# Optimization experiments

Hardware: AMD Instinct MI355X
Metric: run time of the kernel (lower is better)

The kernel has to match this reference:

```python
import jax, jax.numpy as jnp
import numpy as np

DIM = 1024
N_HEADS = 16

def setup_inputs() -> dict:
    key = jax.random.key(0)
    ks = jax.random.split(key, 6)
    s = 1.0 / np.sqrt(DIM)
    return {
        "x": jax.random.normal(ks[0], (2, 2048, DIM), dtype=jnp.float32),
        "Wq": jax.random.normal(ks[1], (DIM, DIM), dtype=jnp.float32) * s,
        "Wk": jax.random.normal(ks[2], (DIM, DIM), dtype=jnp.float32) * s,
        "Wv": jax.random.normal(ks[3], (DIM, DIM), dtype=jnp.float32) * s,
        "Wo": jax.random.normal(ks[4], (DIM, DIM), dtype=jnp.float32) * s,
        "bo": jax.random.normal(ks[5], (DIM,), dtype=jnp.float32) * 0.01,
    }

def reference(x, Wq, Wk, Wv, Wo, bo):
    B, S, D = x.shape
    H = N_HEADS
    hd = D // H
    # linear layers: y = x @ W.T (torch convention)
    def proj(W):
        y = jnp.einsum('bsd,ed->bse', x, W)
        return y.reshape(B, S, H, hd).transpose(0, 2, 1, 3)  # [B,H,S,hd]
    q, k, v = proj(Wq), proj(Wk), proj(Wv)
    attn = jnp.einsum('bhqd,bhkd->bhqk', q, k) / jnp.sqrt(jnp.float32(hd))
    attn = jax.nn.softmax(attn, axis=-1)
    out = jnp.einsum('bhqk,bhkd->bhqd', attn, v)
    out = out.transpose(0, 2, 1, 3).reshape(B, S, D)
    out = jnp.einsum('bsd,ed->bse', out, Wo) + bo
    return out
```

## Files before the change

kernel.cpp:

```cpp
#include <hip/hip_runtime.h>
#include <hip/hip_bf16.h>

#define SEQ 2048
#define DIM 1024
#define NH 16
#define HD 64
#define MTOT 4096

typedef __attribute__((ext_vector_type(8))) short bf16x8;
typedef __attribute__((ext_vector_type(4))) float f32x4;
typedef __attribute__((ext_vector_type(16))) float f32x16;
typedef __attribute__((ext_vector_type(4))) unsigned int u32x4;
typedef __attribute__((ext_vector_type(2))) unsigned int u32x2;

typedef const __attribute__((address_space(1))) void* gptr_t;
typedef __attribute__((address_space(3))) void* sptr_t;

static __device__ __forceinline__ unsigned short f2bf(float f) {
    unsigned int u = __builtin_bit_cast(unsigned int, f);
    return (unsigned short)((u + 0x7FFFu + ((u >> 16) & 1u)) >> 16);
}

#define CVTPK(d, x, y) asm("v_cvt_pk_bf16_f32 %0, %1, %2" : "=v"(d) : "v"(x), "v"(y))
#define PLSWAP(a, b) asm("v_permlane32_swap_b32 %0, %1" : "+v"(a), "+v"(b))

__global__ void cast_kernel(const float* __restrict__ in, unsigned short* __restrict__ out, int n) {
    int i = (blockIdx.x * 256 + threadIdx.x) * 4;
    if (i < n) {
        float4 v = *reinterpret_cast<const float4*>(in + i);
        ushort4 o;
        o.x = f2bf(v.x); o.y = f2bf(v.y); o.z = f2bf(v.z); o.w = f2bf(v.w);
        *reinterpret_cast<ushort4*>(out + i) = o;
    }
}

template<int MODE>
__global__ __launch_bounds__(256) void gemm_nt(
    const unsigned short* __restrict__ A,
    const unsigned short* __restrict__ B0,
    const unsigned short* __restrict__ B1,
    const unsigned short* __restrict__ B2,
    unsigned short* __restrict__ D0,
    unsigned short* __restrict__ D1,
    unsigned short* __restrict__ D2,
    float* __restrict__ Df,
    const float* __restrict__ bias)
{
    constexpr int K = DIM;
    __shared__ __align__(16) unsigned short Asm[128 * 32];
    __shared__ __align__(16) unsigned short Bsm[128 * 32];

    const int tid = threadIdx.x;
    const int wave = tid >> 6, lane = tid & 63;
    const int wm = wave >> 1, wn = wave & 1;
    const int m0 = blockIdx.y * 128, n0 = blockIdx.x * 128;
    const int fr = lane & 15;

    const unsigned short* Bsel = (MODE == 1 || blockIdx.z == 0) ? B0 : (blockIdx.z == 1 ? B1 : B2);

    const int srow = wave * 32 + (lane >> 2);
    const int schunk = (lane & 3) ^ ((lane >> 3) & 3);
    const size_t abase = (size_t)(m0 + srow) * K + (size_t)schunk * 8;
    const size_t bbase = (size_t)(n0 + srow) * K + (size_t)schunk * 8;

    f32x4 acc[4][4] = {};

    for (int k0 = 0; k0 < K; k0 += 32) {
        #pragma unroll
        for (int c = 0; c < 2; ++c) {
            __builtin_amdgcn_global_load_lds(
                (gptr_t)(A + abase + (size_t)c * 16 * K + k0),
                (sptr_t)((char*)Asm + wave * 2048 + c * 1024), 16, 0, 0);
            __builtin_amdgcn_global_load_lds(
                (gptr_t)(Bsel + bbase + (size_t)c * 16 * K + k0),
                (sptr_t)((char*)Bsm + wave * 2048 + c * 1024), 16, 0, 0);
        }
        __syncthreads();

        bf16x8 af[4], bf[4];
        const int ca = ((lane >> 4) ^ ((fr >> 1) & 3)) * 16;
        #pragma unroll
        for (int i = 0; i < 4; ++i) {
            int ra = wm * 64 + i * 16 + fr;
            int rb = wn * 64 + i * 16 + fr;
            af[i] = *(const bf16x8*)((const char*)Asm + ra * 64 + ca);
            bf[i] = *(const bf16x8*)((const char*)Bsm + rb * 64 + ca);
        }
        #pragma unroll
        for (int i = 0; i < 4; ++i)
            #pragma unroll
            for (int j = 0; j < 4; ++j)
                acc[i][j] = __builtin_amdgcn_mfma_f32_16x16x32_bf16(af[i], bf[j], acc[i][j], 0, 0, 0);
        __syncthreads();
    }

    if (MODE == 0) {
        unsigned short* Dst = (blockIdx.z == 0) ? D0 : (blockIdx.z == 1 ? D1 : D2);
        const float scale = (blockIdx.z == 0) ? 0.1803368787f : 1.0f;
        #pragma unroll
        for (int i = 0; i < 4; ++i)
            #pragma unroll
            for (int j = 0; j < 4; ++j)
                #pragma unroll
                for (int r = 0; r < 4; ++r) {
                    int m = m0 + wm * 64 + i * 16 + (lane >> 4) * 4 + r;
                    int n = n0 + wn * 64 + j * 16 + fr;
                    int b = m >> 11, s = m & 2047, h = n >> 6, dh = n & 63;
                    Dst[(((size_t)(b * NH + h)) * SEQ + s) * HD + dh] = f2bf(acc[i][j][r] * scale);
                }
    } else {
        #pragma unroll
        for (int i = 0; i < 4; ++i)
            #pragma unroll
            for (int j = 0; j < 4; ++j)
                #pragma unroll
                for (int r = 0; r < 4; ++r) {
                    int m = m0 + wm * 64 + i * 16 + (lane >> 4) * 4 + r;
                    int n = n0 + wn * 64 + j * 16 + fr;
                    Df[(size_t)m * DIM + n] = acc[i][j][r] + bias[n];
                }
    }
}

__global__ __launch_bounds__(512, 4) void attn_kernel(
    const unsigned short* __restrict__ Q,
    const unsigned short* __restrict__ Kg,
    const unsigned short* __restrict__ Vg,
    float* __restrict__ po,
    float* __restrict__ ml)
{
    __shared__ __align__(16) unsigned short Ksm[2][64 * 66];
    __shared__ __align__(16) unsigned short Vsm[2][64 * 66];

    const int tid = threadIdx.x;
    const int wave = tid >> 6, lane = tid & 63;
    const int lq = lane & 31, hi = lane >> 5;

    const int bid = blockIdx.x;
    const int xcd = bid & 7, slot = bid >> 3;
    const int bh = xcd * 4 + (slot & 3);
    const int rest = slot >> 2;
    const int q0 = (rest >> 1) * 256;
    const int half = rest & 1;
    const int kvbase = half * 1024;

    const unsigned short* Qh = Q + (size_t)bh * SEQ * HD;
    const unsigned short* Kh = Kg + (size_t)bh * SEQ * HD;
    const unsigned short* Vh = Vg + (size_t)bh * SEQ * HD;

    const float MCONST = 12.0f;

    const int qrow = q0 + wave * 32 + lq;
    bf16x8 qf[4];
    #pragma unroll
    for (int dch = 0; dch < 4; ++dch)
        qf[dch] = *(const bf16x8*)(Qh + (size_t)qrow * HD + dch * 16 + hi * 8);

    f32x16 ot0 = {}, ot1 = {};
    float l = 0.f;

    const int krow_s = tid >> 3, kch_s = tid & 7;
    const int kvp_s = tid >> 4, sub_s = tid & 1;
    const int dch_s = (tid >> 1) & 7;

    bf16x8 sk, sv;
    auto stage_load = [&](int t64) {
        sk = *(const bf16x8*)(Kh + (size_t)(t64 + krow_s) * HD + kch_s * 8);
        sv = *(const bf16x8*)(Vh + (size_t)(t64 + 2 * kvp_s + sub_s) * HD + dch_s * 8);
    };
    auto stage_write = [&](int buf) {
        u32x4 kw = __builtin_bit_cast(u32x4, sk);
        unsigned* kp = (unsigned*)((char*)&Ksm[buf][0] + 132 * krow_s + 16 * kch_s);
        kp[0] = kw[0]; kp[1] = kw[1]; kp[2] = kw[2]; kp[3] = kw[3];
        u32x4 vw = __builtin_bit_cast(u32x4, sv);
        unsigned p0 = (unsigned)__shfl_xor((int)vw[0], 1);
        unsigned p1 = (unsigned)__shfl_xor((int)vw[1], 1);
        unsigned p2 = (unsigned)__shfl_xor((int)vw[2], 1);
        unsigned p3 = (unsigned)__shfl_xor((int)vw[3], 1);
        unsigned ea0 = sub_s ? p2 : vw[0];
        unsigned ea1 = sub_s ? p3 : vw[1];
        unsigned eb0 = sub_s ? vw[2] : p0;
        unsigned eb1 = sub_s ? vw[3] : p1;
        unsigned* vp = (unsigned*)&Vsm[buf][0];
        const int dbase = dch_s * 8 + sub_s * 4;
        vp[33 * (dbase + 0) + kvp_s] = (ea0 & 0xffffu) | (eb0 << 16);
        vp[33 * (dbase + 1) + kvp_s] = (ea0 >> 16) | (eb0 & 0xffff0000u);
        vp[33 * (dbase + 2) + kvp_s] = (ea1 & 0xffffu) | (eb1 << 16);
        vp[33 * (dbase + 3) + kvp_s] = (ea1 >> 16) | (eb1 & 0xffff0000u);
    };

    stage_load(kvbase);
    stage_write(0);
    __syncthreads();

    int cur = 0;
    #pragma unroll 1
    for (int t = 0; t < 16; ++t) {
        if (t < 15) stage_load(kvbase + (t + 1) * 64);

        const char* Kb = (const char*)&Ksm[cur][0];
        const char* Vb = (const char*)&Vsm[cur][0];

        f32x16 st0, st1;
        #pragma unroll
        for (int r = 0; r < 16; ++r) { st0[r] = -MCONST; st1[r] = -MCONST; }
        __builtin_amdgcn_s_setprio(1);
        #pragma unroll
        for (int dch = 0; dch < 4; ++dch) {
            const unsigned* a0 = (const unsigned*)(Kb + 132 * lq + 32 * dch + 16 * hi);
            const unsigned* a1 = (const unsigned*)(Kb + 132 * (32 + lq) + 32 * dch + 16 * hi);
            u32x4 f0 = {a0[0], a0[1], a0[2], a0[3]};
            u32x4 f1 = {a1[0], a1[1], a1[2], a1[3]};
            st0 = __builtin_amdgcn_mfma_f32_32x32x16_bf16(__builtin_bit_cast(bf16x8, f0), qf[dch], st0, 0, 0, 0);
            st1 = __builtin_amdgcn_mfma_f32_32x32x16_bf16(__builtin_bit_cast(bf16x8, f1), qf[dch], st1, 0, 0, 0);
        }
        __builtin_amdgcn_s_setprio(0);

        float sa = 0.f, sb = 0.f, sc = 0.f, sd = 0.f;
        #pragma unroll
        for (int r = 0; r < 16; r += 4) {
            st0[r]     = exp2f(st0[r]);     sa += st0[r];
            st0[r + 1] = exp2f(st0[r + 1]); sb += st0[r + 1];
            st0[r + 2] = exp2f(st0[r + 2]); sc += st0[r + 2];
            st0[r + 3] = exp2f(st0[r + 3]); sd += st0[r + 3];
        }
        #pragma unroll
        for (int r = 0; r < 16; r += 4) {
            st1[r]     = exp2f(st1[r]);     sa += st1[r];
            st1[r + 1] = exp2f(st1[r + 1]); sb += st1[r + 1];
            st1[r + 2] = exp2f(st1[r + 2]); sc += st1[r + 2];
            st1[r + 3] = exp2f(st1[r + 3]); sd += st1[r + 3];
        }
        float ps = (sa + sb) + (sc + sd);
        ps += __shfl_xor(ps, 32);
        l += ps;

        bf16x8 pf0, pf1, pf2, pf3;
        {
            unsigned w0, w1, w2, w3, w4, w5, w6, w7;
            CVTPK(w0, st0[0], st0[1]);   CVTPK(w1, st0[2], st0[3]);
            CVTPK(w2, st0[4], st0[5]);   CVTPK(w3, st0[6], st0[7]);
            CVTPK(w4, st0[8], st0[9]);   CVTPK(w5, st0[10], st0[11]);
            CVTPK(w6, st0[12], st0[13]); CVTPK(w7, st0[14], st0[15]);
            PLSWAP(w0, w2); PLSWAP(w1, w3); PLSWAP(w4, w6); PLSWAP(w5, w7);
            u32x4 uA = {w0, w1, w2, w3}, uB = {w4, w5, w6, w7};
            pf0 = __builtin_bit_cast(bf16x8, uA);
            pf1 = __builtin_bit_cast(bf16x8, uB);
        }
        {
            unsigned w0, w1, w2, w3, w4, w5, w6, w7;
            CVTPK(w0, st1[0], st1[1]);   CVTPK(w1, st1[2], st1[3]);
            CVTPK(w2, st1[4], st1[5]);   CVTPK(w3, st1[6], st1[7]);
            CVTPK(w4, st1[8], st1[9]);   CVTPK(w5, st1[10], st1[11]);
            CVTPK(w6, st1[12], st1[13]); CVTPK(w7, st1[14], st1[15]);
            PLSWAP(w0, w2); PLSWAP(w1, w3); PLSWAP(w4, w6); PLSWAP(w5, w7);
            u32x4 uA = {w0, w1, w2, w3}, uB = {w4, w5, w6, w7};
            pf2 = __builtin_bit_cast(bf16x8, uA);
            pf3 = __builtin_bit_cast(bf16x8, uB);
        }

        __builtin_amdgcn_s_setprio(1);
        #pragma unroll
        for (int kc = 0; kc < 4; ++kc) {
            const unsigned* v0 = (const unsigned*)(Vb + 132 * lq + 32 * kc + 16 * hi);
            const unsigned* v1 = (const unsigned*)(Vb + 132 * (32 + lq) + 32 * kc + 16 * hi);
            u32x4 g0 = {v0[0], v0[1], v0[2], v0[3]};
            u32x4 g1 = {v1[0], v1[1], v1[2], v1[3]};
            bf16x8 pfv = (kc == 0) ? pf0 : (kc == 1) ? pf1 : (kc == 2) ? pf2 : pf3;
            ot0 = __builtin_amdgcn_mfma_f32_32x32x16_bf16(__builtin_bit_cast(bf16x8, g0), pfv, ot0, 0, 0, 0);
            ot1 = __builtin_amdgcn_mfma_f32_32x32x16_bf16(__builtin_bit_cast(bf16x8, g1), pfv, ot1, 0, 0, 0);
        }
        __builtin_amdgcn_s_setprio(0);

        if (t < 15) stage_write(cur ^ 1);
        __syncthreads();
        cur ^= 1;
    }

    const size_t prow = (size_t)(half * 32 + bh) * SEQ + qrow;
    float* por = po + prow * 64;
    #pragma unroll
    for (int tg = 0; tg < 4; ++tg) {
        f32x4 v0 = {ot0[4 * tg + 0], ot0[4 * tg + 1], ot0[4 * tg + 2], ot0[4 * tg + 3]};
        *(f32x4*)(por + 8 * tg + 4 * hi) = v0;
        f32x4 v1 = {ot1[4 * tg + 0], ot1[4 * tg + 1], ot1[4 * tg + 2], ot1[4 * tg + 3]};
        *(f32x4*)(por + 32 + 8 * tg + 4 * hi) = v1;
    }
    if (hi == 0) ml[prow] = l;
}

__global__ __launch_bounds__(256) void merge_kernel(
    const float* __restrict__ po,
    const float* __restrict__ ml,
    unsigned short* __restrict__ ob)
{
    const int gid = blockIdx.x * 256 + threadIdx.x;
    const int row = gid >> 3, dch = gid & 7;
    const size_t p1 = row, p2 = (size_t)32 * SEQ + row;
    const float inv = 1.0f / (ml[p1] + ml[p2]);

    f32x4 a0 = *(const f32x4*)(po + p1 * 64 + dch * 8);
    f32x4 a1 = *(const f32x4*)(po + p1 * 64 + dch * 8 + 4);
    f32x4 b0 = *(const f32x4*)(po + p2 * 64 + dch * 8);
    f32x4 b1 = *(const f32x4*)(po + p2 * 64 + dch * 8 + 4);

    unsigned wA, wB, wC, wD;
    CVTPK(wA, (a0[0] + b0[0]) * inv, (a0[1] + b0[1]) * inv);
    CVTPK(wB, (a0[2] + b0[2]) * inv, (a0[3] + b0[3]) * inv);
    CVTPK(wC, (a1[0] + b1[0]) * inv, (a1[1] + b1[1]) * inv);
    CVTPK(wD, (a1[2] + b1[2]) * inv, (a1[3] + b1[3]) * inv);
    u32x4 w = {wA, wB, wC, wD};

    const int bh = row >> 11, s = row & 2047;
    const int b = bh >> 4, h = bh & 15;
    *(u32x4*)(ob + ((size_t)(b * SEQ + s)) * DIM + h * HD + dch * 8) = w;
}

extern "C" void kernel_launch(void* const* d_in, const int* in_sizes, int n_in,
                              void* d_out, int out_size, void* d_ws, size_t ws_size,
                              hipStream_t stream) {
    const float* x  = (const float*)d_in[0];
    const float* Wq = (const float*)d_in[1];
    const float* Wk = (const float*)d_in[2];
    const float* Wv = (const float*)d_in[3];
    const float* Wo = (const float*)d_in[4];
    const float* bo = (const float*)d_in[5];
    float* out = (float*)d_out;

    unsigned short* ws = (unsigned short*)d_ws;
    unsigned short* xb  = ws;
    unsigned short* wqb = xb + (size_t)MTOT * DIM;
    unsigned short* wkb = wqb + (size_t)DIM * DIM;
    unsigned short* wvb = wkb + (size_t)DIM * DIM;
    unsigned short* wob = wvb + (size_t)DIM * DIM;
    unsigned short* qb  = wob + (size_t)DIM * DIM;
    unsigned short* kb  = qb + (size_t)MTOT * DIM;
    unsigned short* vb  = kb + (size_t)MTOT * DIM;
    unsigned short* ob  = vb + (size_t)MTOT * DIM;
    float* po = (float*)(ob + (size_t)MTOT * DIM);
    float* ml = po + (size_t)2 * 32 * SEQ * 64;

    cast_kernel<<<dim3(MTOT * DIM / 1024), 256, 0, stream>>>(x, xb, MTOT * DIM);
    cast_kernel<<<dim3(DIM * DIM / 1024), 256, 0, stream>>>(Wq, wqb, DIM * DIM);
    cast_kernel<<<dim3(DIM * DIM / 1024), 256, 0, stream>>>(Wk, wkb, DIM * DIM);
    cast_kernel<<<dim3(DIM * DIM / 1024), 256, 0, stream>>>(Wv, wvb, DIM * DIM);
    cast_kernel<<<dim3(DIM * DIM / 1024), 256, 0, stream>>>(Wo, wob, DIM * DIM);

    gemm_nt<0><<<dim3(DIM / 128, MTOT / 128, 3), 256, 0, stream>>>(
        xb, wqb, wkb, wvb, qb, kb, vb, nullptr, nullptr);

    attn_kernel<<<dim3(512), 512, 0, stream>>>(qb, kb, vb, po, ml);

    merge_kernel<<<dim3(2048), 256, 0, stream>>>(po, ml, ob);

    gemm_nt<1><<<dim3(DIM / 128, MTOT / 128, 1), 256, 0, stream>>>(
        ob, wob, nullptr, nullptr, nullptr, nullptr, nullptr, out, bo);
}
```

Before: 144.8 us.

## Process two query row tiles per wave to reuse K/V fragments

Each attention wave now handles 64 query rows (two 32-row tiles) instead of 32, reusing the K and V fragments read from shared memory for both tiles. The grid is halved to 256 blocks with 512-row query chunks, and the launch bound's occupancy hint is lowered to fit the higher register use. This reduces LDS and global K/V traffic per unit of matrix work. The cost is lower occupancy, with only one block per CU, and heavier register pressure.

```diff
diff --git a/kernel.cpp b/kernel.cpp
--- a/kernel.cpp
+++ b/kernel.cpp
@@ -122,7 +122,7 @@
     }
 }
 
-__global__ __launch_bounds__(512, 4) void attn_kernel(
+__global__ __launch_bounds__(512, 2) void attn_kernel(
     const unsigned short* __restrict__ Q,
     const unsigned short* __restrict__ Kg,
     const unsigned short* __restrict__ Vg,
@@ -140,7 +140,7 @@
     const int xcd = bid & 7, slot = bid >> 3;
     const int bh = xcd * 4 + (slot & 3);
     const int rest = slot >> 2;
-    const int q0 = (rest >> 1) * 256;
+    const int q0 = (rest >> 1) * 512;
     const int half = rest & 1;
     const int kvbase = half * 1024;
 
@@ -150,14 +150,17 @@
 
     const float MCONST = 12.0f;
 
-    const int qrow = q0 + wave * 32 + lq;
-    bf16x8 qf[4];
+    const int qrowA = q0 + wave * 64 + lq;
+    const int qrowB = qrowA + 32;
+    bf16x8 qfA[4], qfB[4];
     #pragma unroll
-    for (int dch = 0; dch < 4; ++dch)
-        qf[dch] = *(const bf16x8*)(Qh + (size_t)qrow * HD + dch * 16 + hi * 8);
-
-    f32x16 ot0 = {}, ot1 = {};
-    float l = 0.f;
+    for (int dch = 0; dch < 4; ++dch) {
+        qfA[dch] = *(const bf16x8*)(Qh + (size_t)qrowA * HD + dch * 16 + hi * 8);
+        qfB[dch] = *(const bf16x8*)(Qh + (size_t)qrowB * HD + dch * 16 + hi * 8);
+    }
+
+    f32x16 oA0 = {}, oA1 = {}, oB0 = {}, oB1 = {};
+    float lA = 0.f, lB = 0.f;
 
     const int krow_s = tid >> 3, kch_s = tid & 7;
     const int kvp_s = tid >> 4, sub_s = tid & 1;
@@ -201,62 +204,113 @@
         const char* Kb = (const char*)&Ksm[cur][0];
         const char* Vb = (const char*)&Vsm[cur][0];
 
-        f32x16 st0, st1;
-        #pragma unroll
-        for (int r = 0; r < 16; ++r) { st0[r] = -MCONST; st1[r] = -MCONST; }
-        __builtin_amdgcn_s_setprio(1);
+        bf16x8 kf0[4], kf1[4];
         #pragma unroll
         for (int dch = 0; dch < 4; ++dch) {
             const unsigned* a0 = (const unsigned*)(Kb + 132 * lq + 32 * dch + 16 * hi);
             const unsigned* a1 = (const unsigned*)(Kb + 132 * (32 + lq) + 32 * dch + 16 * hi);
             u32x4 f0 = {a0[0], a0[1], a0[2], a0[3]};
             u32x4 f1 = {a1[0], a1[1], a1[2], a1[3]};
-            st0 = __builtin_amdgcn_mfma_f32_32x32x16_bf16(__builtin_bit_cast(bf16x8, f0), qf[dch], st0, 0, 0, 0);
-            st1 = __builtin_amdgcn_mfma_f32_32x32x16_bf16(__builtin_bit_cast(bf16x8, f1), qf[dch], st1, 0, 0, 0);
-        }
-        __builtin_amdgcn_s_setprio(0);
-
-        float sa = 0.f, sb = 0.f, sc = 0.f, sd = 0.f;
-        #pragma unroll
-        for (int r = 0; r < 16; r += 4) {
-            st0[r]     = exp2f(st0[r]);     sa += st0[r];
-            st0[r + 1] = exp2f(st0[r + 1]); sb += st0[r + 1];
-            st0[r + 2] = exp2f(st0[r + 2]); sc += st0[r + 2];
-            st0[r + 3] = exp2f(st0[r + 3]); sd += st0[r + 3];
-        }
-        #pragma unroll
-        for (int r = 0; r < 16; r += 4) {
-            st1[r]     = exp2f(st1[r]);     sa += st1[r];
-            st1[r + 1] = exp2f(st1[r + 1]); sb += st1[r + 1];
-            st1[r + 2] = exp2f(st1[r + 2]); sc += st1[r + 2];
-            st1[r + 3] = exp2f(st1[r + 3]); sd += st1[r + 3];
-        }
-        float ps = (sa + sb) + (sc + sd);
-        ps += __shfl_xor(ps, 32);
-        l += ps;
-
-        bf16x8 pf0, pf1, pf2, pf3;
+            kf0[dch] = __builtin_bit_cast(bf16x8, f0);
+            kf1[dch] = __builtin_bit_cast(bf16x8, f1);
+        }
+
+        bf16x8 pfA[4], pfB[4];
+
         {
+            f32x16 s0, s1;
+            #pragma unroll
+            for (int r = 0; r < 16; ++r) { s0[r] = -MCONST; s1[r] = -MCONST; }
+            __builtin_amdgcn_s_setprio(1);
+            #pragma unroll
+            for (int dch = 0; dch < 4; ++dch) {
+                s0 = __builtin_amdgcn_mfma_f32_32x32x16_bf16(kf0[dch], qfA[dch], s0, 0, 0, 0);
+                s1 = __builtin_amdgcn_mfma_f32_32x32x16_bf16(kf1[dch], qfA[dch], s1, 0, 0, 0);
+            }
+            __builtin_amdgcn_s_setprio(0);
+            float sa = 0.f, sb = 0.f, sc = 0.f, sd = 0.f;
+            #pragma unroll
+            for (int r = 0; r < 16; r += 4) {
+                s0[r]     = exp2f(s0[r]);     sa += s0[r];
+                s0[r + 1] = exp2f(s0[r + 1]); sb += s0[r + 1];
+                s0[r + 2] = exp2f(s0[r + 2]); sc += s0[r + 2];
+                s0[r + 3] = exp2f(s0[r + 3]); sd += s0[r + 3];
+            }
+            #pragma unroll
+            for (int r = 0; r < 16; r += 4) {
+                s1[r]     = exp2f(s1[r]);     sa += s1[r];
+                s1[r + 1] = exp2f(s1[r + 1]); sb += s1[r + 1];
+                s1[r + 2] = exp2f(s1[r + 2]); sc += s1[r + 2];
+                s1[r + 3] = exp2f(s1[r + 3]); sd += s1[r + 3];
+            }
+            float ps = (sa + sb) + (sc + sd);
+            ps += __shfl_xor(ps, 32);
+            lA += ps;
             unsigned w0, w1, w2, w3, w4, w5, w6, w7;
-            CVTPK(w0, st0[0], st0[1]);   CVTPK(w1, st0[2], st0[3]);
-            CVTPK(w2, st0[4], st0[5]);   CVTPK(w3, st0[6], st0[7]);
-            CVTPK(w4, st0[8], st0[9]);   CVTPK(w5, st0[10], st0[11]);
-            CVTPK(w6, st0[12], st0[13]); CVTPK(w7, st0[14], st0[15]);
+            CVTPK(w0, s0[0], s0[1]);   CVTPK(w1, s0[2], s0[3]);
+            CVTPK(w2, s0[4], s0[5]);   CVTPK(w3, s0[6], s0[7]);
+            CVTPK(w4, s0[8], s0[9]);   CVTPK(w5, s0[10], s0[11]);
+            CVTPK(w6, s0[12], s0[13]); CVTPK(w7, s0[14], s0[15]);
             PLSWAP(w0, w2); PLSWAP(w1, w3); PLSWAP(w4, w6); PLSWAP(w5, w7);
             u32x4 uA = {w0, w1, w2, w3}, uB = {w4, w5, w6, w7};
-            pf0 = __builtin_bit_cast(bf16x8, uA);
-            pf1 = __builtin_bit_cast(bf16x8, uB);
-        }
+            pfA[0] = __builtin_bit_cast(bf16x8, uA);
+            pfA[1] = __builtin_bit_cast(bf16x8, uB);
+            CVTPK(w0, s1[0], s1[1]);   CVTPK(w1, s1[2], s1[3]);
+            CVTPK(w2, s1[4], s1[5]);   CVTPK(w3, s1[6], s1[7]);
+            CVTPK(w4, s1[8], s1[9]);   CVTPK(w5, s1[10], s1[11]);
+            CVTPK(w6, s1[12], s1[13]); CVTPK(w7, s1[14], s1[15]);
+            PLSWAP(w0, w2); PLSWAP(w1, w3); PLSWAP(w4, w6); PLSWAP(w5, w7);
+            u32x4 uC = {w0, w1, w2, w3}, uD = {w4, w5, w6, w7};
+            pfA[2] = __builtin_bit_cast(bf16x8, uC);
+            pfA[3] = __builtin_bit_cast(bf16x8, uD);
+        }
+
         {
+            f32x16 s0, s1;
+            #pragma unroll
+            for (int r = 0; r < 16; ++r) { s0[r] = -MCONST; s1[r] = -MCONST; }
+            __builtin_amdgcn_s_setprio(1);
+            #pragma unroll
+            for (int dch = 0; dch < 4; ++dch) {
+                s0 = __builtin_amdgcn_mfma_f32_32x32x16_bf16(kf0[dch], qfB[dch], s0, 0, 0, 0);
+                s1 = __builtin_amdgcn_mfma_f32_32x32x16_bf16(kf1[dch], qfB[dch], s1, 0, 0, 0);
+            }
+            __builtin_amdgcn_s_setprio(0);
+            float sa = 0.f, sb = 0.f, sc = 0.f, sd = 0.f;
+            #pragma unroll
+            for (int r = 0; r < 16; r += 4) {
+                s0[r]     = exp2f(s0[r]);     sa += s0[r];
+                s0[r + 1] = exp2f(s0[r + 1]); sb += s0[r + 1];
+                s0[r + 2] = exp2f(s0[r + 2]); sc += s0[r + 2];
+                s0[r + 3] = exp2f(s0[r + 3]); sd += s0[r + 3];
+            }
+            #pragma unroll
+            for (int r = 0; r < 16; r += 4) {
+                s1[r]     = exp2f(s1[r]);     sa += s1[r];
+                s1[r + 1] = exp2f(s1[r + 1]); sb += s1[r + 1];
+                s1[r + 2] = exp2f(s1[r + 2]); sc += s1[r + 2];
+                s1[r + 3] = exp2f(s1[r + 3]); sd += s1[r + 3];
+            }
+            float ps = (sa + sb) + (sc + sd);
+            ps += __shfl_xor(ps, 32);
+            lB += ps;
             unsigned w0, w1, w2, w3, w4, w5, w6, w7;
-            CVTPK(w0, st1[0], st1[1]);   CVTPK(w1, st1[2], st1[3]);
-            CVTPK(w2, st1[4], st1[5]);   CVTPK(w3, st1[6], st1[7]);
-            CVTPK(w4, st1[8], st1[9]);   CVTPK(w5, st1[10], st1[11]);
-            CVTPK(w6, st1[12], st1[13]); CVTPK(w7, st1[14], st1[15]);
+            CVTPK(w0, s0[0], s0[1]);   CVTPK(w1, s0[2], s0[3]);
+            CVTPK(w2, s0[4], s0[5]);   CVTPK(w3, s0[6], s0[7]);
+            CVTPK(w4, s0[8], s0[9]);   CVTPK(w5, s0[10], s0[11]);
+            CVTPK(w6, s0[12], s0[13]); CVTPK(w7, s0[14], s0[15]);
             PLSWAP(w0, w2); PLSWAP(w1, w3); PLSWAP(w4, w6); PLSWAP(w5, w7);
             u32x4 uA = {w0, w1, w2, w3}, uB = {w4, w5, w6, w7};
-            pf2 = __builtin_bit_cast(bf16x8, uA);
-            pf3 = __builtin_bit_cast(bf16x8, uB);
+            pfB[0] = __builtin_bit_cast(bf16x8, uA);
+            pfB[1] = __builtin_bit_cast(bf16x8, uB);
+            CVTPK(w0, s1[0], s1[1]);   CVTPK(w1, s1[2], s1[3]);
+            CVTPK(w2, s1[4], s1[5]);   CVTPK(w3, s1[6], s1[7]);
+            CVTPK(w4, s1[8], s1[9]);   CVTPK(w5, s1[10], s1[11]);
+            CVTPK(w6, s1[12], s1[13]); CVTPK(w7, s1[14], s1[15]);
+            PLSWAP(w0, w2); PLSWAP(w1, w3); PLSWAP(w4, w6); PLSWAP(w5, w7);
+            u32x4 uC = {w0, w1, w2, w3}, uD = {w4, w5, w6, w7};
+            pfB[2] = __builtin_bit_cast(bf16x8, uC);
+            pfB[3] = __builtin_bit_cast(bf16x8, uD);
         }
 
         __builtin_amdgcn_s_setprio(1);
@@ -266,9 +320,12 @@
             const unsigned* v1 = (const unsigned*)(Vb + 132 * (32 + lq) + 32 * kc + 16 * hi);
             u32x4 g0 = {v0[0], v0[1], v0[2], v0[3]};
             u32x4 g1 = {v1[0], v1[1], v1[2], v1[3]};
-            bf16x8 pfv = (kc == 0) ? pf0 : (kc == 1) ? pf1 : (kc == 2) ? pf2 : pf3;
-            ot0 = __builtin_amdgcn_mfma_f32_32x32x16_bf16(__builtin_bit_cast(bf16x8, g0), pfv, ot0, 0, 0, 0);
-            ot1 = __builtin_amdgcn_mfma_f32_32x32x16_bf16(__builtin_bit_cast(bf16x8, g1), pfv, ot1, 0, 0, 0);
+            bf16x8 vf0 = __builtin_bit_cast(bf16x8, g0);
+            bf16x8 vf1 = __builtin_bit_cast(bf16x8, g1);
+            oA0 = __builtin_amdgcn_mfma_f32_32x32x16_bf16(vf0, pfA[kc], oA0, 0, 0, 0);
+            oA1 = __builtin_amdgcn_mfma_f32_32x32x16_bf16(vf1, pfA[kc], oA1, 0, 0, 0);
+            oB0 = __builtin_amdgcn_mfma_f32_32x32x16_bf16(vf0, pfB[kc], oB0, 0, 0, 0);
+            oB1 = __builtin_amdgcn_mfma_f32_32x32x16_bf16(vf1, pfB[kc], oB1, 0, 0, 0);
         }
         __builtin_amdgcn_s_setprio(0);
 
@@ -277,16 +334,22 @@
         cur ^= 1;
     }
 
-    const size_t prow = (size_t)(half * 32 + bh) * SEQ + qrow;
-    float* por = po + prow * 64;
+    const size_t prowA = (size_t)(half * 32 + bh) * SEQ + qrowA;
+    const size_t prowB = (size_t)(half * 32 + bh) * SEQ + qrowB;
+    float* porA = po + prowA * 64;
+    float* porB = po + prowB * 64;
     #pragma unroll
     for (int tg = 0; tg < 4; ++tg) {
-        f32x4 v0 = {ot0[4 * tg + 0], ot0[4 * tg + 1], ot0[4 * tg + 2], ot0[4 * tg + 3]};
-        *(f32x4*)(por + 8 * tg + 4 * hi) = v0;
-        f32x4 v1 = {ot1[4 * tg + 0], ot1[4 * tg + 1], ot1[4 * tg + 2], ot1[4 * tg + 3]};
-        *(f32x4*)(por + 32 + 8 * tg + 4 * hi) = v1;
-    }
-    if (hi == 0) ml[prow] = l;
+        f32x4 a0 = {oA0[4 * tg + 0], oA0[4 * tg + 1], oA0[4 * tg + 2], oA0[4 * tg + 3]};
+        *(f32x4*)(porA + 8 * tg + 4 * hi) = a0;
+        f32x4 a1 = {oA1[4 * tg + 0], oA1[4 * tg + 1], oA1[4 * tg + 2], oA1[4 * tg + 3]};
+        *(f32x4*)(porA + 32 + 8 * tg + 4 * hi) = a1;
+        f32x4 b0 = {oB0[4 * tg + 0], oB0[4 * tg + 1], oB0[4 * tg + 2], oB0[4 * tg + 3]};
+        *(f32x4*)(porB + 8 * tg + 4 * hi) = b0;
+        f32x4 b1 = {oB1[4 * tg + 0], oB1[4 * tg + 1], oB1[4 * tg + 2], oB1[4 * tg + 3]};
+        *(f32x4*)(porB + 32 + 8 * tg + 4 * hi) = b1;
+    }
+    if (hi == 0) { ml[prowA] = lA; ml[prowB] = lB; }
 }
 
 __global__ __launch_bounds__(256) void merge_kernel(
@@ -349,7 +412,7 @@
     gemm_nt<0><<<dim3(DIM / 128, MTOT / 128, 3), 256, 0, stream>>>(
         xb, wqb, wkb, wvb, qb, kb, vb, nullptr, nullptr);
 
-    attn_kernel<<<dim3(512), 512, 0, stream>>>(qb, kb, vb, po, ml);
+    attn_kernel<<<dim3(256), 512, 0, stream>>>(qb, kb, vb, po, ml);
 
     merge_kernel<<<dim3(2048), 256, 0, stream>>>(po, ml, ob);
 
```

Result: slower. 156.6 us (+8.1%).
